# Kernel tuning notes

Hardware: AMD Instinct MI355X
Metric: run time of the kernel (lower is better)

Reference implementation:

```python
import jax, jax.numpy as jnp
import numpy as np

B, S, D_MODEL = 2, 4096, 1024
H_Q, D_K = 8, 64
H_IDX, D_IDX = 2, 32
TOP_K = 256
LN_EPS = 1e-5


def setup_inputs() -> dict:
    key = jax.random.key(0)
    ks = jax.random.split(key, 12)
    inp = {
        "x": jax.random.normal(ks[0], (B, S, D_MODEL), jnp.float32),
        "Q": jax.random.normal(ks[1], (B, H_Q, S, D_K), jnp.float32),
        "K": jax.random.normal(ks[2], (B, S, D_K), jnp.float32),
        "V": jax.random.normal(ks[3], (B, S, D_K), jnp.float32),
        # indexer params
        "Wq_idx": jax.random.normal(ks[4], (H_IDX * D_IDX, D_MODEL), jnp.float32) * 0.02,
        "bq_idx": jnp.zeros((H_IDX * D_IDX,), jnp.float32),
        "Wk_idx": jax.random.normal(ks[5], (H_IDX * D_IDX, D_MODEL), jnp.float32) * 0.02,
        "bk_idx": jnp.zeros((H_IDX * D_IDX,), jnp.float32),
        "ln_g": jnp.ones((D_IDX,), jnp.float32),
        "ln_b": jnp.zeros((D_IDX,), jnp.float32),
        "idx_w": jnp.full((H_IDX,), 0.1, jnp.float32),
    }
    return inp


def _layernorm(t, g, b):
    m = jnp.mean(t, axis=-1, keepdims=True)
    v = jnp.var(t, axis=-1, keepdims=True)
    return (t - m) * jax.lax.rsqrt(v + LN_EPS) * g + b


def reference(x, Q, K, V, Wq_idx, bq_idx, Wk_idx, bk_idx, ln_g, ln_b, idx_w):
    b, s, _ = x.shape
    dk = Q.shape[-1]
    # indexer projections -> [B,S,H_idx,D_idx]
    q_i = (x @ Wq_idx.T + bq_idx).reshape(b, s, H_IDX, D_IDX)
    k_i = (x @ Wk_idx.T + bk_idx).reshape(b, s, H_IDX, D_IDX)
    q_i = _layernorm(q_i, ln_g, ln_b)
    k_i = _layernorm(k_i, ln_g, ln_b)
    # pairwise indexer scores (faithful to torch einsum order): [B,H_idx,S,S]
    head_scores = jax.nn.relu(jnp.einsum('bshd,bthd->bhst', k_i, q_i))
    index_scores = jnp.einsum('bhst,h->bst', head_scores, idx_w)  # [B,S,S]
    top_k = min(TOP_K, s)
    _, top_idx = jax.lax.top_k(index_scores, top_k)  # [B,S,top_k]
    # gather per-query K/V: [B,S,top_k,d_k]
    K_topk = jnp.take_along_axis(K[:, None, :, :], top_idx[..., None], axis=2)
    V_topk = jnp.take_along_axis(V[:, None, :, :], top_idx[..., None], axis=2)
    Qr = jnp.transpose(Q, (0, 2, 1, 3))  # [B,S,H,d_k]
    scale = 1.0 / jnp.sqrt(jnp.asarray(dk, Q.dtype))
    attn = jnp.einsum('bshd,bskd->bshk', Qr, K_topk) * scale  # [B,S,H,top_k]
    w = jax.nn.softmax(attn, axis=-1)  # dropout is identity in eval mode
    out = jnp.einsum('bshk,bskd->bshd', w, V_topk)
    return out.reshape(b, s, -1)  # [B,S,H*d_k]; kl_loss==0 in sparse phase
```

## Files before the change

### kernel.cpp

```cpp
#include <hip/hip_runtime.h>
#include <math.h>


#define B_   2
#define S_   4096
#define DM_  1024
#define HQ_  8
#define TK_  256

typedef unsigned int u32;
typedef unsigned long long u64;
typedef unsigned short US;
typedef __attribute__((ext_vector_type(8))) short short8;
typedef __attribute__((ext_vector_type(4))) float f32x4;

__device__ __forceinline__ float dot4(const float4 a, const float4 b) {
    return a.x*b.x + a.y*b.y + a.z*b.z + a.w*b.w;
}
__device__ __forceinline__ u32 fkey(float f) {
    u32 b = __float_as_uint(f);
    return (b & 0x80000000u) ? ~b : (b | 0x80000000u);
}
__device__ __forceinline__ u32 bfbits(float f) {
    const u32 u = __float_as_uint(f);
    return (u + 0x7FFFu + ((u >> 16) & 1u)) >> 16;
}
__device__ __forceinline__ float bfval(u32 bits) {
    return __uint_as_float(bits << 16);
}

__global__ __launch_bounds__(256) void k_proj_ln(
    const float* __restrict__ x,
    const float* __restrict__ Wq, const float* __restrict__ bq,
    const float* __restrict__ Wk, const float* __restrict__ bk,
    const float* __restrict__ lg, const float* __restrict__ lb,
    US* __restrict__ qa, US* __restrict__ qb, US* __restrict__ qc,
    US* __restrict__ ka, US* __restrict__ kb, US* __restrict__ kc)
{
    __shared__ float xs[16*64];
    const int tid = threadIdx.x;
    const int o   = tid & 63;
    const int rh  = tid >> 6;
    const size_t r0 = (size_t)blockIdx.x * 16;

    float acc[2][4];
    #pragma unroll
    for (int j = 0; j < 2; ++j)
        #pragma unroll
        for (int r = 0; r < 4; ++r) acc[j][r] = 0.f;

    const float* wqr = Wq + (size_t)o * DM_;
    const float* wkr = Wk + (size_t)o * DM_;

    for (int kt = 0; kt < 16; ++kt) {
        {
            const int row = tid >> 4, c4 = (tid & 15) << 2;
            *(float4*)&xs[row*64 + c4] =
                *(const float4*)&x[(r0 + row) * DM_ + kt*64 + c4];
        }
        __syncthreads();
        #pragma unroll
        for (int k8 = 0; k8 < 8; ++k8) {
            const int base = kt*64 + k8*8;
            const float4 wq0 = *(const float4*)&wqr[base];
            const float4 wq1 = *(const float4*)&wqr[base+4];
            const float4 wk0 = *(const float4*)&wkr[base];
            const float4 wk1 = *(const float4*)&wkr[base+4];
            #pragma unroll
            for (int rr = 0; rr < 4; ++rr) {
                const float* xr = &xs[(rh*4+rr)*64 + k8*8];
                const float4 xa = *(const float4*)xr;
                const float4 xb = *(const float4*)(xr+4);
                acc[0][rr] += dot4(wq0,xa) + dot4(wq1,xb);
                acc[1][rr] += dot4(wk0,xa) + dot4(wk1,xb);
            }
        }
        __syncthreads();
    }

    const float bqv = bq[o], bkv = bk[o];
    const float gv = lg[o & 31], bv = lb[o & 31];
    #pragma unroll
    for (int j = 0; j < 2; ++j) {
        #pragma unroll
        for (int rr = 0; rr < 4; ++rr) {
            float v = acc[j][rr] + (j == 0 ? bqv : bkv);
            float s = v;
            #pragma unroll
            for (int off = 16; off >= 1; off >>= 1) s += __shfl_xor(s, off, 32);
            const float m = s * (1.f/32.f);
            const float d = v - m;
            float s2 = d * d;
            #pragma unroll
            for (int off = 16; off >= 1; off >>= 1) s2 += __shfl_xor(s2, off, 32);
            const float var = s2 * (1.f/32.f);
            const float ov = d * rsqrtf(var + 1e-5f) * gv + bv;
            const size_t idx = (r0 + rh*4 + rr)*64 + o;
            const u32 ab = bfbits(ov);
            const float fa = bfval(ab);
            const float r1 = ov - fa;
            const u32 bb = bfbits(r1);
            const float fb = bfval(bb);
            const u32 cb = bfbits(r1 - fb);
            if (j == 0) { qa[idx] = (US)ab; qb[idx] = (US)bb; qc[idx] = (US)cb; }
            else        { ka[idx] = (US)ab; kb[idx] = (US)bb; kc[idx] = (US)cb; }
        }
    }
}

__global__ __launch_bounds__(256) void k_scores_mfma(
    const US* __restrict__ qa, const US* __restrict__ qb, const US* __restrict__ qc,
    const US* __restrict__ ka, const US* __restrict__ kb, const US* __restrict__ kc,
    const float* __restrict__ idxw, u32* __restrict__ keys)
{
    const int tid  = threadIdx.x;
    const int w    = tid >> 6, lane = tid & 63;
    const int row16 = lane & 15, kblk = lane >> 4;
    const int b    = blockIdx.y >> 6;
    const int sB   = (blockIdx.y & 63)*64 + (w >> 1)*32;
    const int tB   = blockIdx.x*64 + (w & 1)*32;
    const float w0 = idxw[0], w1 = idxw[1];

    const US* kL[3] = { ka, kb, kc };
    const US* qL[3] = { qa, qb, qc };

    const size_t sOff = ((size_t)b*S_ + sB + row16)*64 + (size_t)kblk*8;
    const size_t tOff = ((size_t)b*S_ + tB + row16)*64 + (size_t)kblk*8;

    short8 A[2][2][3], Bv[2][2][3];
    #pragma unroll
    for (int st = 0; st < 2; ++st)
        #pragma unroll
        for (int h = 0; h < 2; ++h)
            #pragma unroll
            for (int l = 0; l < 3; ++l) {
                A[st][h][l]  = *(const short8*)(kL[l] + sOff + st*1024 + h*32);
                Bv[st][h][l] = *(const short8*)(qL[l] + tOff + st*1024 + h*32);
            }

    #pragma unroll
    for (int st = 0; st < 2; ++st) {
        #pragma unroll
        for (int tt = 0; tt < 2; ++tt) {
            f32x4 acc[2];
            #pragma unroll
            for (int h = 0; h < 2; ++h) {
                f32x4 c = {0.f, 0.f, 0.f, 0.f};
                c = __builtin_amdgcn_mfma_f32_16x16x32_bf16(A[st][h][1], Bv[tt][h][1], c, 0,0,0);
                c = __builtin_amdgcn_mfma_f32_16x16x32_bf16(A[st][h][0], Bv[tt][h][2], c, 0,0,0);
                c = __builtin_amdgcn_mfma_f32_16x16x32_bf16(A[st][h][2], Bv[tt][h][0], c, 0,0,0);
                c = __builtin_amdgcn_mfma_f32_16x16x32_bf16(A[st][h][0], Bv[tt][h][1], c, 0,0,0);
                c = __builtin_amdgcn_mfma_f32_16x16x32_bf16(A[st][h][1], Bv[tt][h][0], c, 0,0,0);
                c = __builtin_amdgcn_mfma_f32_16x16x32_bf16(A[st][h][0], Bv[tt][h][0], c, 0,0,0);
                acc[h] = c;
            }
            u32* kout = keys + ((size_t)b*S_ + sB + st*16 + kblk*4)*S_
                             + tB + tt*16 + row16;
            #pragma unroll
            for (int r = 0; r < 4; ++r) {
                const float sc = w0*fmaxf(acc[0][r], 0.f) + w1*fmaxf(acc[1][r], 0.f);
                kout[(size_t)r*S_] = fkey(sc);
            }
        }
    }
}

__global__ __launch_bounds__(256) void k_select(
    const u32* __restrict__ keys, int* __restrict__ top)
{
    __shared__ u32 kly[4096];
    __shared__ u32 hist[4][256];
    __shared__ u32 wcnt[8];

    const int tid = threadIdx.x, lane = tid & 63, w = tid >> 6;
    const size_t row = blockIdx.x;
    const u32* krow = keys + row * S_;

    #pragma unroll
    for (int i = 0; i < 4; ++i)
        ((uint4*)kly)[tid + i*256] = ((const uint4*)krow)[tid + i*256];
    __syncthreads();

    u32 prefix = 0; u32 krem = TK_;
    #pragma unroll 1
    for (int pass = 0; pass < 4; ++pass) {
        const int shift = 24 - 8*pass;
        ((uint4*)hist)[tid] = make_uint4(0u,0u,0u,0u);
        __syncthreads();
        #pragma unroll
        for (int i = 0; i < 16; ++i) {
            const u32 kk = kly[tid + i*256];
            const bool ok = (pass == 0) | ((kk >> (shift+8)) == prefix);
            if (ok) atomicAdd(&hist[w][(kk >> shift) & 255], 1u);
        }
        __syncthreads();
        const uint4 t0 = ((const uint4*)hist[0])[lane];
        const uint4 t1 = ((const uint4*)hist[1])[lane];
        const uint4 t2 = ((const uint4*)hist[2])[lane];
        const uint4 t3 = ((const uint4*)hist[3])[lane];
        uint4 h4;
        h4.x = t0.x + t1.x + t2.x + t3.x;
        h4.y = t0.y + t1.y + t2.y + t3.y;
        h4.z = t0.z + t1.z + t2.z + t3.z;
        h4.w = t0.w + t1.w + t2.w + t3.w;
        u32 ssum = h4.x + h4.y + h4.z + h4.w;
        #pragma unroll
        for (int off = 1; off < 64; off <<= 1) {
            const u32 tt = __shfl_down(ssum, off);
            if (lane + off < 64) ssum += tt;
        }
        u32 up = __shfl_down(ssum, 1);
        if (lane == 63) up = 0;
        const u32 a3 = up;
        const u32 a2 = a3 + h4.w;
        const u32 a1 = a2 + h4.z;
        const u32 a0 = a1 + h4.y;
        u32 binl = 0, nkl = 0; bool hit = false;
        if      (a0 < krem && a0 + h4.x >= krem) { hit = true; binl = 4*lane+0; nkl = krem - a0; }
        else if (a1 < krem && a1 + h4.y >= krem) { hit = true; binl = 4*lane+1; nkl = krem - a1; }
        else if (a2 < krem && a2 + h4.z >= krem) { hit = true; binl = 4*lane+2; nkl = krem - a2; }
        else if (a3 < krem && a3 + h4.w >= krem) { hit = true; binl = 4*lane+3; nkl = krem - a3; }
        const u64 mball = __ballot(hit);
        const int src = __ffsll(mball) - 1;
        const u32 bsel = __shfl(binl, src);
        krem = __shfl(nkl, src);
        prefix = (prefix << 8) | bsel;
        __syncthreads();
    }

    const u32 T = prefix;
    const int G = TK_ - (int)krem;
    const u64 lmask = (lane == 0) ? 0ull : ((~0ull) >> (64 - lane));
    int cgt = 0, ceq = 0;
    #pragma unroll
    for (int i = 0; i < 16; ++i) {
        const u32 kk = kly[w*1024 + i*64 + lane];
        cgt += __popcll(__ballot(kk > T));
        ceq += __popcll(__ballot(kk == T));
    }
    if (lane == 0) { wcnt[w] = (u32)cgt; wcnt[4 + w] = (u32)ceq; }
    __syncthreads();
    int gts = 0, eqs = 0;
    for (int w2 = 0; w2 < 4; ++w2) {
        if (w2 < w) { gts += (int)wcnt[w2]; eqs += (int)wcnt[4 + w2]; }
    }
    int* orow = top + row * TK_;
    cgt = gts; ceq = eqs;
    #pragma unroll
    for (int i = 0; i < 16; ++i) {
        const int idx = w*1024 + i*64 + lane;
        const u32 kk = kly[idx];
        const bool gt = kk > T, eq = kk == T;
        const u64 mgt = __ballot(gt), meq = __ballot(eq);
        if (gt) orow[cgt + __popcll(mgt & lmask)] = idx;
        if (eq) {
            const int rk = ceq + __popcll(meq & lmask);
            if (rk < (int)krem) orow[G + rk] = idx;
        }
        cgt += __popcll(mgt); ceq += __popcll(meq);
    }
}

__global__ __launch_bounds__(256) void k_attn(
    const float* __restrict__ Q, const float* __restrict__ K,
    const float* __restrict__ V, const int* __restrict__ top,
    float* __restrict__ out)
{
    __shared__ int   il[256];
    __shared__ float qsm[8*64];
    __shared__ float wmat[8*256];
    __shared__ float opart[4*8*64];
    __shared__ float MZ[16];

    const int tid  = threadIdx.x;
    const int b    = blockIdx.x >> 12;
    const int s    = blockIdx.x & 4095;
    const int lane = tid & 63, w = tid >> 6;

    il[tid] = top[((size_t)(b*S_ + s))*TK_ + tid];
    qsm[tid]     = Q[((size_t)(b*HQ_ + (tid>>6)))*S_*64 + (size_t)s*64 + (tid&63)];
    qsm[256+tid] = Q[((size_t)(b*HQ_ + 4 + (tid>>6)))*S_*64 + (size_t)s*64 + (tid&63)];
    __syncthreads();

    const float* kp = K + ((size_t)(b*S_ + il[tid]))*64;
    float4 kx[16];
    #pragma unroll
    for (int g = 0; g < 16; ++g) kx[g] = *(const float4*)(kp + g*4);
    float sc[8];
    #pragma unroll
    for (int h = 0; h < 8; ++h) {
        float a = 0.f;
        #pragma unroll
        for (int g = 0; g < 16; ++g)
            a += dot4(*(const float4*)&qsm[h*64 + g*4], kx[g]);
        sc[h] = a * 0.125f;
    }
    #pragma unroll
    for (int h = 0; h < 8; ++h) wmat[h*256 + tid] = sc[h];
    __syncthreads();

    #pragma unroll
    for (int hh = 0; hh < 2; ++hh) {
        const int h = hh*4 + w;
        const float4 v4 = *(const float4*)&wmat[h*256 + lane*4];
        float mm = fmaxf(fmaxf(v4.x, v4.y), fmaxf(v4.z, v4.w));
        #pragma unroll
        for (int off = 32; off >= 1; off >>= 1) mm = fmaxf(mm, __shfl_xor(mm, off));
        if (lane == 0) MZ[h] = mm;
    }
    __syncthreads();
    #pragma unroll
    for (int h = 0; h < 8; ++h) wmat[h*256 + tid] = __expf(sc[h] - MZ[h]);
    __syncthreads();
    #pragma unroll
    for (int hh = 0; hh < 2; ++hh) {
        const int h = hh*4 + w;
        const float4 v4 = *(const float4*)&wmat[h*256 + lane*4];
        float ss = v4.x + v4.y + v4.z + v4.w;
        #pragma unroll
        for (int off = 32; off >= 1; off >>= 1) ss += __shfl_xor(ss, off);
        if (lane == 0) MZ[8 + h] = ss;
    }
    __syncthreads();

    const int dq = lane & 15, jsub = lane >> 4;
    float4 p[8];
    #pragma unroll
    for (int h = 0; h < 8; ++h) p[h] = make_float4(0.f,0.f,0.f,0.f);
    #pragma unroll
    for (int i = 0; i < 16; ++i) {
        const int j = w*64 + jsub*16 + i;
        const float4 v4 = *(const float4*)&V[((size_t)(b*S_ + il[j]))*64 + dq*4];
        #pragma unroll
        for (int h = 0; h < 8; ++h) {
            const float wv = wmat[h*256 + j];
            p[h].x += wv*v4.x; p[h].y += wv*v4.y;
            p[h].z += wv*v4.z; p[h].w += wv*v4.w;
        }
    }
    #pragma unroll
    for (int h = 0; h < 8; ++h) {
        p[h].x += __shfl_xor(p[h].x, 16); p[h].y += __shfl_xor(p[h].y, 16);
        p[h].z += __shfl_xor(p[h].z, 16); p[h].w += __shfl_xor(p[h].w, 16);
        p[h].x += __shfl_xor(p[h].x, 32); p[h].y += __shfl_xor(p[h].y, 32);
        p[h].z += __shfl_xor(p[h].z, 32); p[h].w += __shfl_xor(p[h].w, 32);
    }
    if (jsub == 0) {
        #pragma unroll
        for (int h = 0; h < 8; ++h)
            *(float4*)&opart[(w*8 + h)*64 + dq*4] = p[h];
    }
    __syncthreads();
    {
        const int h = tid >> 5, d0 = (tid & 31) * 2;
        float o0 = 0.f, o1 = 0.f;
        #pragma unroll
        for (int g = 0; g < 4; ++g) {
            o0 += opart[(g*8 + h)*64 + d0];
            o1 += opart[(g*8 + h)*64 + d0 + 1];
        }
        const float iz = 1.f / MZ[8 + h];
        *(float2*)&out[((size_t)(b*S_ + s))*512 + h*64 + d0] =
            make_float2(o0*iz, o1*iz);
    }
}

extern "C" void kernel_launch(void* const* d_in, const int* in_sizes, int n_in,
                              void* d_out, int out_size, void* d_ws, size_t ws_size,
                              hipStream_t stream) {
    const float* x  = (const float*)d_in[0];
    const float* Q  = (const float*)d_in[1];
    const float* K  = (const float*)d_in[2];
    const float* V  = (const float*)d_in[3];
    const float* Wq = (const float*)d_in[4];
    const float* bq = (const float*)d_in[5];
    const float* Wk = (const float*)d_in[6];
    const float* bk = (const float*)d_in[7];
    const float* lg = (const float*)d_in[8];
    const float* lb = (const float*)d_in[9];
    const float* iw = (const float*)d_in[10];
    float* out = (float*)d_out;

    char* ws = (char*)d_ws;
    int*  top = (int*)ws;
    US*   qa  = (US*)(ws + ( 8u<<20));
    US*   qb  = (US*)(ws + ( 9u<<20));
    US*   qc  = (US*)(ws + (10u<<20));
    US*   ka  = (US*)(ws + (11u<<20));
    US*   kb  = (US*)(ws + (12u<<20));
    US*   kc  = (US*)(ws + (13u<<20));
    u32* keys = (u32*)(ws + (16u<<20));

    (void)in_sizes; (void)n_in; (void)out_size; (void)ws_size;

    k_proj_ln<<<dim3((B_*S_)/16), dim3(256), 0, stream>>>(
        x, Wq, bq, Wk, bk, lg, lb, qa, qb, qc, ka, kb, kc);
    k_scores_mfma<<<dim3(S_/64, (B_*S_)/64), dim3(256), 0, stream>>>(
        qa, qb, qc, ka, kb, kc, iw, keys);
    k_select<<<dim3(B_*S_), dim3(256), 0, stream>>>(keys, top);
    k_attn<<<dim3(B_*S_), dim3(256), 0, stream>>>(
        Q, K, V, top, out);
}
```

Measured before the change: 540.1 us.

## Move indexer projection to split-bf16 MFMA and fuse top-k select with attention

Replaces the FP32 scalar projection+layernorm with a kernel that splits x and the weights into three bf16 limbs and uses six MFMA products per tile, with a separate pre-pass splitting the weights. Layernorm now uses a single-pass sum/sum-of-squares reduction. The radix top-k select and sparse attention are merged into one kernel that writes indices to shared memory, removing the top-index global round trip and one launch. This adds an extra weight-split launch and slightly changes numerics through the variance formula and truncated bf16 cross terms.

After: 459.4 us. -14.9%, faster.

```diff
diff --git a/kernel.cpp b/kernel.cpp
--- a/kernel.cpp
+++ b/kernel.cpp
@@ -28,83 +28,131 @@
 __device__ __forceinline__ float bfval(u32 bits) {
     return __uint_as_float(bits << 16);
 }
-
-__global__ __launch_bounds__(256) void k_proj_ln(
-    const float* __restrict__ x,
-    const float* __restrict__ Wq, const float* __restrict__ bq,
-    const float* __restrict__ Wk, const float* __restrict__ bk,
+__device__ __forceinline__ void split3(float v, US& a, US& b, US& c) {
+    const u32 ab = bfbits(v); const float fa = bfval(ab);
+    const float r1 = v - fa;
+    const u32 bb = bfbits(r1); const float fb = bfval(bb);
+    const u32 cb = bfbits(r1 - fb);
+    a = (US)ab; b = (US)bb; c = (US)cb;
+}
+
+__global__ __launch_bounds__(256) void k_wsplit(
+    const float* __restrict__ Wq, const float* __restrict__ Wk,
+    US* __restrict__ wl)
+{
+    const int o   = blockIdx.x;
+    const int tid = threadIdx.x;
+    const float* src = (o < 64) ? (Wq + (size_t)o*DM_)
+                                : (Wk + (size_t)(o-64)*DM_);
+    const int k0 = tid * 4;
+    const float4 v = *(const float4*)&src[k0];
+    float vv[4] = {v.x, v.y, v.z, v.w};
+    US aa[4], bb[4], cc[4];
+    #pragma unroll
+    for (int i = 0; i < 4; ++i) split3(vv[i], aa[i], bb[i], cc[i]);
+    const size_t base = (size_t)o*DM_ + k0;
+    *(ushort4*)&wl[0*131072 + base] = make_ushort4(aa[0],aa[1],aa[2],aa[3]);
+    *(ushort4*)&wl[1*131072 + base] = make_ushort4(bb[0],bb[1],bb[2],bb[3]);
+    *(ushort4*)&wl[2*131072 + base] = make_ushort4(cc[0],cc[1],cc[2],cc[3]);
+}
+
+__global__ __launch_bounds__(256) void k_proj_mfma(
+    const float* __restrict__ x, const US* __restrict__ wl,
+    const float* __restrict__ bq, const float* __restrict__ bk,
     const float* __restrict__ lg, const float* __restrict__ lb,
     US* __restrict__ qa, US* __restrict__ qb, US* __restrict__ qc,
     US* __restrict__ ka, US* __restrict__ kb, US* __restrict__ kc)
 {
-    __shared__ float xs[16*64];
-    const int tid = threadIdx.x;
-    const int o   = tid & 63;
-    const int rh  = tid >> 6;
-    const size_t r0 = (size_t)blockIdx.x * 16;
-
-    float acc[2][4];
-    #pragma unroll
-    for (int j = 0; j < 2; ++j)
-        #pragma unroll
-        for (int r = 0; r < 4; ++r) acc[j][r] = 0.f;
-
-    const float* wqr = Wq + (size_t)o * DM_;
-    const float* wkr = Wk + (size_t)o * DM_;
-
-    for (int kt = 0; kt < 16; ++kt) {
+    __shared__ US xl[3][16][264];
+    const int tid   = threadIdx.x;
+    const int w     = tid >> 6, lane = tid & 63;
+    const int row16 = lane & 15, kblk = lane >> 4;
+    const size_t s0 = (size_t)blockIdx.x * 16;
+
+    f32x4 acc0 = {0.f,0.f,0.f,0.f};
+    f32x4 acc1 = {0.f,0.f,0.f,0.f};
+
+    const int srow = tid >> 4;
+    const int scol = (tid & 15) * 16;
+
+    for (int ck = 0; ck < 4; ++ck) {
         {
-            const int row = tid >> 4, c4 = (tid & 15) << 2;
-            *(float4*)&xs[row*64 + c4] =
-                *(const float4*)&x[(r0 + row) * DM_ + kt*64 + c4];
+            const float* xr = x + (s0 + srow)*DM_ + ck*256 + scol;
+            #pragma unroll
+            for (int q4 = 0; q4 < 4; ++q4) {
+                const float4 v = *(const float4*)(xr + q4*4);
+                float vv[4] = {v.x, v.y, v.z, v.w};
+                US aa[4], bb[4], cc[4];
+                #pragma unroll
+                for (int i = 0; i < 4; ++i) split3(vv[i], aa[i], bb[i], cc[i]);
+                const int cb = scol + q4*4;
+                *(ushort4*)&xl[0][srow][cb] = make_ushort4(aa[0],aa[1],aa[2],aa[3]);
+                *(ushort4*)&xl[1][srow][cb] = make_ushort4(bb[0],bb[1],bb[2],bb[3]);
+                *(ushort4*)&xl[2][srow][cb] = make_ushort4(cc[0],cc[1],cc[2],cc[3]);
+            }
         }
         __syncthreads();
         #pragma unroll
-        for (int k8 = 0; k8 < 8; ++k8) {
-            const int base = kt*64 + k8*8;
-            const float4 wq0 = *(const float4*)&wqr[base];
-            const float4 wq1 = *(const float4*)&wqr[base+4];
-            const float4 wk0 = *(const float4*)&wkr[base];
-            const float4 wk1 = *(const float4*)&wkr[base+4];
-            #pragma unroll
-            for (int rr = 0; rr < 4; ++rr) {
-                const float* xr = &xs[(rh*4+rr)*64 + k8*8];
-                const float4 xa = *(const float4*)xr;
-                const float4 xb = *(const float4*)(xr+4);
-                acc[0][rr] += dot4(wq0,xa) + dot4(wq1,xb);
-                acc[1][rr] += dot4(wk0,xa) + dot4(wk1,xb);
-            }
+        for (int kt = 0; kt < 8; ++kt) {
+            short8 A[3], B0[3], B1[3];
+            #pragma unroll
+            for (int l = 0; l < 3; ++l)
+                A[l] = *(const short8*)&xl[l][row16][kt*32 + kblk*8];
+            const size_t wko = (size_t)(ck*256 + kt*32 + kblk*8);
+            #pragma unroll
+            for (int l = 0; l < 3; ++l) {
+                B0[l] = *(const short8*)&wl[(size_t)l*131072 + (size_t)(w*32 +      row16)*DM_ + wko];
+                B1[l] = *(const short8*)&wl[(size_t)l*131072 + (size_t)(w*32 + 16 + row16)*DM_ + wko];
+            }
+            acc0 = __builtin_amdgcn_mfma_f32_16x16x32_bf16(A[1], B0[1], acc0, 0,0,0);
+            acc0 = __builtin_amdgcn_mfma_f32_16x16x32_bf16(A[0], B0[2], acc0, 0,0,0);
+            acc0 = __builtin_amdgcn_mfma_f32_16x16x32_bf16(A[2], B0[0], acc0, 0,0,0);
+            acc0 = __builtin_amdgcn_mfma_f32_16x16x32_bf16(A[0], B0[1], acc0, 0,0,0);
+            acc0 = __builtin_amdgcn_mfma_f32_16x16x32_bf16(A[1], B0[0], acc0, 0,0,0);
+            acc0 = __builtin_amdgcn_mfma_f32_16x16x32_bf16(A[0], B0[0], acc0, 0,0,0);
+            acc1 = __builtin_amdgcn_mfma_f32_16x16x32_bf16(A[1], B1[1], acc1, 0,0,0);
+            acc1 = __builtin_amdgcn_mfma_f32_16x16x32_bf16(A[0], B1[2], acc1, 0,0,0);
+            acc1 = __builtin_amdgcn_mfma_f32_16x16x32_bf16(A[2], B1[0], acc1, 0,0,0);
+            acc1 = __builtin_amdgcn_mfma_f32_16x16x32_bf16(A[0], B1[1], acc1, 0,0,0);
+            acc1 = __builtin_amdgcn_mfma_f32_16x16x32_bf16(A[1], B1[0], acc1, 0,0,0);
+            acc1 = __builtin_amdgcn_mfma_f32_16x16x32_bf16(A[0], B1[0], acc1, 0,0,0);
         }
         __syncthreads();
     }
 
-    const float bqv = bq[o], bkv = bk[o];
-    const float gv = lg[o & 31], bv = lb[o & 31];
-    #pragma unroll
-    for (int j = 0; j < 2; ++j) {
-        #pragma unroll
-        for (int rr = 0; rr < 4; ++rr) {
-            float v = acc[j][rr] + (j == 0 ? bqv : bkv);
-            float s = v;
-            #pragma unroll
-            for (int off = 16; off >= 1; off >>= 1) s += __shfl_xor(s, off, 32);
-            const float m = s * (1.f/32.f);
-            const float d = v - m;
-            float s2 = d * d;
-            #pragma unroll
-            for (int off = 16; off >= 1; off >>= 1) s2 += __shfl_xor(s2, off, 32);
-            const float var = s2 * (1.f/32.f);
-            const float ov = d * rsqrtf(var + 1e-5f) * gv + bv;
-            const size_t idx = (r0 + rh*4 + rr)*64 + o;
-            const u32 ab = bfbits(ov);
-            const float fa = bfval(ab);
-            const float r1 = ov - fa;
-            const u32 bb = bfbits(r1);
-            const float fb = bfval(bb);
-            const u32 cb = bfbits(r1 - fb);
-            if (j == 0) { qa[idx] = (US)ab; qb[idx] = (US)bb; qc[idx] = (US)cb; }
-            else        { ka[idx] = (US)ab; kb[idx] = (US)bb; kc[idx] = (US)cb; }
-        }
+    const int c0 = w*32 + row16;
+    const int c1 = c0 + 16;
+    const float bias0 = (w < 2) ? bq[c0] : bk[c0 - 64];
+    const float bias1 = (w < 2) ? bq[c1] : bk[c1 - 64];
+    const float gv0 = lg[c0 & 31], bv0 = lb[c0 & 31];
+    const float gv1 = lg[c1 & 31], bv1 = lb[c1 & 31];
+    US* __restrict__ oa = (w < 2) ? qa : ka;
+    US* __restrict__ ob = (w < 2) ? qb : kb;
+    US* __restrict__ oc = (w < 2) ? qc : kc;
+    const int oc0 = c0 & 63, oc1 = c1 & 63;
+
+    #pragma unroll
+    for (int r = 0; r < 4; ++r) {
+        const float v0 = acc0[r] + bias0;
+        const float v1 = acc1[r] + bias1;
+        float s1 = v0 + v1;
+        float s2 = v0*v0 + v1*v1;
+        #pragma unroll
+        for (int off = 1; off < 16; off <<= 1) {
+            s1 += __shfl_xor(s1, off);
+            s2 += __shfl_xor(s2, off);
+        }
+        const float m   = s1 * (1.f/32.f);
+        const float var = fmaxf(s2 * (1.f/32.f) - m*m, 0.f);
+        const float inv = rsqrtf(var + 1e-5f);
+        const float o0 = (v0 - m)*inv*gv0 + bv0;
+        const float o1 = (v1 - m)*inv*gv1 + bv1;
+        const size_t grow = s0 + (size_t)kblk*4 + r;
+        US a0,b0,cl0, a1,b1,cl1;
+        split3(o0, a0, b0, cl0);
+        split3(o1, a1, b1, cl1);
+        oa[grow*64 + oc0] = a0; ob[grow*64 + oc0] = b0; oc[grow*64 + oc0] = cl0;
+        oa[grow*64 + oc1] = a1; ob[grow*64 + oc1] = b1; oc[grow*64 + oc1] = cl1;
     }
 }
 
@@ -165,119 +213,114 @@
     }
 }
 
-__global__ __launch_bounds__(256) void k_select(
-    const u32* __restrict__ keys, int* __restrict__ top)
+__global__ __launch_bounds__(256) void k_sel_attn(
+    const u32* __restrict__ keys,
+    const float* __restrict__ Q, const float* __restrict__ K,
+    const float* __restrict__ V, float* __restrict__ out)
 {
-    __shared__ u32 kly[4096];
-    __shared__ u32 hist[4][256];
-    __shared__ u32 wcnt[8];
+    __shared__ __align__(16) char smemraw[20480];
+    __shared__ u32  wcnt[8];
+    __shared__ int  il[256];
+    __shared__ float MZ[16];
+
+    u32* kly  = (u32*)smemraw;
+    u32* hist = (u32*)(smemraw + 16384);
 
     const int tid = threadIdx.x, lane = tid & 63, w = tid >> 6;
     const size_t row = blockIdx.x;
-    const u32* krow = keys + row * S_;
-
-    #pragma unroll
-    for (int i = 0; i < 4; ++i)
-        ((uint4*)kly)[tid + i*256] = ((const uint4*)krow)[tid + i*256];
-    __syncthreads();
-
-    u32 prefix = 0; u32 krem = TK_;
-    #pragma unroll 1
-    for (int pass = 0; pass < 4; ++pass) {
-        const int shift = 24 - 8*pass;
-        ((uint4*)hist)[tid] = make_uint4(0u,0u,0u,0u);
+    const int b = (int)(row >> 12);
+    const int s = (int)(row & 4095);
+
+    {
+        const u32* krow = keys + row * S_;
+        #pragma unroll
+        for (int i = 0; i < 4; ++i)
+            ((uint4*)kly)[tid + i*256] = ((const uint4*)krow)[tid + i*256];
         __syncthreads();
+
+        u32 prefix = 0; u32 krem = TK_;
+        #pragma unroll 1
+        for (int pass = 0; pass < 4; ++pass) {
+            const int shift = 24 - 8*pass;
+            ((uint4*)hist)[tid] = make_uint4(0u,0u,0u,0u);
+            __syncthreads();
+            #pragma unroll
+            for (int i = 0; i < 16; ++i) {
+                const u32 kk = kly[tid + i*256];
+                const bool ok = (pass == 0) | ((kk >> (shift+8)) == prefix);
+                if (ok) atomicAdd(&hist[w*256 + ((kk >> shift) & 255)], 1u);
+            }
+            __syncthreads();
+            const uint4 t0 = ((const uint4*)(hist      ))[lane];
+            const uint4 t1 = ((const uint4*)(hist + 256))[lane];
+            const uint4 t2 = ((const uint4*)(hist + 512))[lane];
+            const uint4 t3 = ((const uint4*)(hist + 768))[lane];
+            uint4 h4;
+            h4.x = t0.x + t1.x + t2.x + t3.x;
+            h4.y = t0.y + t1.y + t2.y + t3.y;
+            h4.z = t0.z + t1.z + t2.z + t3.z;
+            h4.w = t0.w + t1.w + t2.w + t3.w;
+            u32 ssum = h4.x + h4.y + h4.z + h4.w;
+            #pragma unroll
+            for (int off = 1; off < 64; off <<= 1) {
+                const u32 tt = __shfl_down(ssum, off);
+                if (lane + off < 64) ssum += tt;
+            }
+            u32 up = __shfl_down(ssum, 1);
+            if (lane == 63) up = 0;
+            const u32 a3 = up;
+            const u32 a2 = a3 + h4.w;
+            const u32 a1 = a2 + h4.z;
+            const u32 a0 = a1 + h4.y;
+            u32 binl = 0, nkl = 0; bool hit = false;
+            if      (a0 < krem && a0 + h4.x >= krem) { hit = true; binl = 4*lane+0; nkl = krem - a0; }
+            else if (a1 < krem && a1 + h4.y >= krem) { hit = true; binl = 4*lane+1; nkl = krem - a1; }
+            else if (a2 < krem && a2 + h4.z >= krem) { hit = true; binl = 4*lane+2; nkl = krem - a2; }
+            else if (a3 < krem && a3 + h4.w >= krem) { hit = true; binl = 4*lane+3; nkl = krem - a3; }
+            const u64 mball = __ballot(hit);
+            const int src = __ffsll(mball) - 1;
+            const u32 bsel = __shfl(binl, src);
+            krem = __shfl(nkl, src);
+            prefix = (prefix << 8) | bsel;
+            __syncthreads();
+        }
+
+        const u32 T = prefix;
+        const int G = TK_ - (int)krem;
+        const u64 lmask = (lane == 0) ? 0ull : ((~0ull) >> (64 - lane));
+        int cgt = 0, ceq = 0;
         #pragma unroll
         for (int i = 0; i < 16; ++i) {
-            const u32 kk = kly[tid + i*256];
-            const bool ok = (pass == 0) | ((kk >> (shift+8)) == prefix);
-            if (ok) atomicAdd(&hist[w][(kk >> shift) & 255], 1u);
-        }
+            const u32 kk = kly[w*1024 + i*64 + lane];
+            cgt += __popcll(__ballot(kk > T));
+            ceq += __popcll(__ballot(kk == T));
+        }
+        if (lane == 0) { wcnt[w] = (u32)cgt; wcnt[4 + w] = (u32)ceq; }
         __syncthreads();
-        const uint4 t0 = ((const uint4*)hist[0])[lane];
-        const uint4 t1 = ((const uint4*)hist[1])[lane];
-        const uint4 t2 = ((const uint4*)hist[2])[lane];
-        const uint4 t3 = ((const uint4*)hist[3])[lane];
-        uint4 h4;
-        h4.x = t0.x + t1.x + t2.x + t3.x;
-        h4.y = t0.y + t1.y + t2.y + t3.y;
-        h4.z = t0.z + t1.z + t2.z + t3.z;
-        h4.w = t0.w + t1.w + t2.w + t3.w;
-        u32 ssum = h4.x + h4.y + h4.z + h4.w;
-        #pragma unroll
-        for (int off = 1; off < 64; off <<= 1) {
-            const u32 tt = __shfl_down(ssum, off);
-            if (lane + off < 64) ssum += tt;
-        }
-        u32 up = __shfl_down(ssum, 1);
-        if (lane == 63) up = 0;
-        const u32 a3 = up;
-        const u32 a2 = a3 + h4.w;
-        const u32 a1 = a2 + h4.z;
-        const u32 a0 = a1 + h4.y;
-        u32 binl = 0, nkl = 0; bool hit = false;
-        if      (a0 < krem && a0 + h4.x >= krem) { hit = true; binl = 4*lane+0; nkl = krem - a0; }
-        else if (a1 < krem && a1 + h4.y >= krem) { hit = true; binl = 4*lane+1; nkl = krem - a1; }
-        else if (a2 < krem && a2 + h4.z >= krem) { hit = true; binl = 4*lane+2; nkl = krem - a2; }
-        else if (a3 < krem && a3 + h4.w >= krem) { hit = true; binl = 4*lane+3; nkl = krem - a3; }
-        const u64 mball = __ballot(hit);
-        const int src = __ffsll(mball) - 1;
-        const u32 bsel = __shfl(binl, src);
-        krem = __shfl(nkl, src);
-        prefix = (prefix << 8) | bsel;
-        __syncthreads();
-    }
-
-    const u32 T = prefix;
-    const int G = TK_ - (int)krem;
-    const u64 lmask = (lane == 0) ? 0ull : ((~0ull) >> (64 - lane));
-    int cgt = 0, ceq = 0;
-    #pragma unroll
-    for (int i = 0; i < 16; ++i) {
-        const u32 kk = kly[w*1024 + i*64 + lane];
-        cgt += __popcll(__ballot(kk > T));
-        ceq += __popcll(__ballot(kk == T));
-    }
-    if (lane == 0) { wcnt[w] = (u32)cgt; wcnt[4 + w] = (u32)ceq; }
-    __syncthreads();
-    int gts = 0, eqs = 0;
-    for (int w2 = 0; w2 < 4; ++w2) {
-        if (w2 < w) { gts += (int)wcnt[w2]; eqs += (int)wcnt[4 + w2]; }
-    }
-    int* orow = top + row * TK_;
-    cgt = gts; ceq = eqs;
-    #pragma unroll
-    for (int i = 0; i < 16; ++i) {
-        const int idx = w*1024 + i*64 + lane;
-        const u32 kk = kly[idx];
-        const bool gt = kk > T, eq = kk == T;
-        const u64 mgt = __ballot(gt), meq = __ballot(eq);
-        if (gt) orow[cgt + __popcll(mgt & lmask)] = idx;
-        if (eq) {
-            const int rk = ceq + __popcll(meq & lmask);
-            if (rk < (int)krem) orow[G + rk] = idx;
-        }
-        cgt += __popcll(mgt); ceq += __popcll(meq);
-    }
-}
-
-__global__ __launch_bounds__(256) void k_attn(
-    const float* __restrict__ Q, const float* __restrict__ K,
-    const float* __restrict__ V, const int* __restrict__ top,
-    float* __restrict__ out)
-{
-    __shared__ int   il[256];
-    __shared__ float qsm[8*64];
-    __shared__ float wmat[8*256];
-    __shared__ float opart[4*8*64];
-    __shared__ float MZ[16];
-
-    const int tid  = threadIdx.x;
-    const int b    = blockIdx.x >> 12;
-    const int s    = blockIdx.x & 4095;
-    const int lane = tid & 63, w = tid >> 6;
-
-    il[tid] = top[((size_t)(b*S_ + s))*TK_ + tid];
+        int gts = 0, eqs = 0;
+        for (int w2 = 0; w2 < 4; ++w2)
+            if (w2 < w) { gts += (int)wcnt[w2]; eqs += (int)wcnt[4 + w2]; }
+        cgt = gts; ceq = eqs;
+        #pragma unroll
+        for (int i = 0; i < 16; ++i) {
+            const int idx = w*1024 + i*64 + lane;
+            const u32 kk = kly[idx];
+            const bool gt = kk > T, eq = kk == T;
+            const u64 mgt = __ballot(gt), meq = __ballot(eq);
+            if (gt) il[cgt + __popcll(mgt & lmask)] = idx;
+            if (eq) {
+                const int rk = ceq + __popcll(meq & lmask);
+                if (rk < (int)krem) il[G + rk] = idx;
+            }
+            cgt += __popcll(mgt); ceq += __popcll(meq);
+        }
+    }
+    __syncthreads();
+
+    float* qsm   = (float*)smemraw;
+    float* wmat  = qsm + 512;
+    float* opart = qsm + 2560;
+
     qsm[tid]     = Q[((size_t)(b*HQ_ + (tid>>6)))*S_*64 + (size_t)s*64 + (tid&63)];
     qsm[256+tid] = Q[((size_t)(b*HQ_ + 4 + (tid>>6)))*S_*64 + (size_t)s*64 + (tid&63)];
     __syncthreads();
@@ -382,22 +425,22 @@
     float* out = (float*)d_out;
 
     char* ws = (char*)d_ws;
-    int*  top = (int*)ws;
-    US*   qa  = (US*)(ws + ( 8u<<20));
-    US*   qb  = (US*)(ws + ( 9u<<20));
-    US*   qc  = (US*)(ws + (10u<<20));
-    US*   ka  = (US*)(ws + (11u<<20));
-    US*   kb  = (US*)(ws + (12u<<20));
-    US*   kc  = (US*)(ws + (13u<<20));
+    US*   wl  = (US*)ws;
+    US*   qa  = (US*)(ws + ( 1u<<20));
+    US*   qb  = (US*)(ws + ( 2u<<20));
+    US*   qc  = (US*)(ws + ( 3u<<20));
+    US*   ka  = (US*)(ws + ( 4u<<20));
+    US*   kb  = (US*)(ws + ( 5u<<20));
+    US*   kc  = (US*)(ws + ( 6u<<20));
     u32* keys = (u32*)(ws + (16u<<20));
 
     (void)in_sizes; (void)n_in; (void)out_size; (void)ws_size;
 
-    k_proj_ln<<<dim3((B_*S_)/16), dim3(256), 0, stream>>>(
-        x, Wq, bq, Wk, bk, lg, lb, qa, qb, qc, ka, kb, kc);
+    k_wsplit<<<dim3(128), dim3(256), 0, stream>>>(Wq, Wk, wl);
+    k_proj_mfma<<<dim3((B_*S_)/16), dim3(256), 0, stream>>>(
+        x, wl, bq, bk, lg, lb, qa, qb, qc, ka, kb, kc);
     k_scores_mfma<<<dim3(S_/64, (B_*S_)/64), dim3(256), 0, stream>>>(
         qa, qb, qc, ka, kb, kc, iw, keys);
-    k_select<<<dim3(B_*S_), dim3(256), 0, stream>>>(keys, top);
-    k_attn<<<dim3(B_*S_), dim3(256), 0, stream>>>(
-        Q, K, V, top, out);
-}
+    k_sel_attn<<<dim3(B_*S_), dim3(256), 0, stream>>>(
+        keys, Q, K, V, out);
+}
```
